# Kernel tuning notes

Measured on AMD Instinct MI355X. Metric: run time of the kernel, lower is better.

## Reference

```python
import jax, jax.numpy as jnp
import numpy as np

B, L, H, NH = 2, 2048, 1024, 16
HD = H // NH  # head dim = 64


def setup_inputs() -> dict:
    key = jax.random.key(0)
    ks = jax.random.split(key, 8)
    s = 0.02  # small init scale for weights
    return {
        "q": jax.random.normal(ks[0], (B, L, H), jnp.float32),
        "k": jax.random.normal(ks[1], (B, L, H), jnp.float32),
        "v": jax.random.normal(ks[2], (B, L, H), jnp.float32),
        "attention_mask": jnp.zeros((B, NH, L, L), jnp.float32),
        "Wq": jax.random.normal(ks[3], (H, H), jnp.float32) * s,
        "bq": jnp.zeros((H,), jnp.float32),
        "Wk": jax.random.normal(ks[4], (H, H), jnp.float32) * s,
        "bk": jnp.zeros((H,), jnp.float32),
        "Wv": jax.random.normal(ks[5], (H, H), jnp.float32) * s,
        "bv": jnp.zeros((H,), jnp.float32),
        "Wo": jax.random.normal(ks[6], (H, H), jnp.float32) * s,
        "bo": jnp.zeros((H,), jnp.float32),
    }


def reference(q, k, v, attention_mask, Wq, bq, Wk, bk, Wv, bv, Wo, bo):
    # Conv1D (GPT-2 style) projections: x @ W + b
    query = q @ Wq + bq  # [B, L, H]
    key = k @ Wk + bk
    value = v @ Wv + bv
    # split heads -> [B, NH, L, HD]
    qh = query.reshape(B, L, NH, HD).transpose(0, 2, 1, 3)
    kh = key.reshape(B, L, NH, HD).transpose(0, 2, 1, 3)
    vh = value.reshape(B, L, NH, HD).transpose(0, 2, 1, 3)
    # scores: [B, NH, L, L]
    w = jnp.einsum("bhqd,bhkd->bhqk", qh, kh) / jnp.sqrt(jnp.float32(HD))
    w = w + attention_mask
    w = jax.nn.softmax(w, axis=-1)  # dropout p=0 -> identity
    out = jnp.einsum("bhqk,bhkd->bhqd", w, vh)  # [B, NH, L, HD]
    # merge heads -> [B, L, H]
    out = out.transpose(0, 2, 1, 3).reshape(B, L, H)
    return out @ Wo + bo
```

## Files before the change

kernel.cpp:

```cpp
#include <hip/hip_runtime.h>

#define NBATCH 2
#define LSEQ   2048
#define NH     16
#define HD     64
#define HDIM   1024
#define MTOK   4096

typedef unsigned short u16;
typedef __attribute__((ext_vector_type(8))) short bf16x8;
typedef __attribute__((ext_vector_type(4))) float f32x4;

__device__ __forceinline__ u16 f2bf(float f) {
  union { float f; unsigned int u; } x; x.f = f;
  return (u16)((x.u + 0x7fffu + ((x.u >> 16) & 1u)) >> 16);
}

__device__ __forceinline__ void gload_lds16(const void* g, void* l) {
  __builtin_amdgcn_global_load_lds(
      (const __attribute__((address_space(1))) unsigned int*)g,
      (__attribute__((address_space(3))) unsigned int*)l, 16, 0, 0);
}

__global__ void prep_kernel(
    const float* __restrict__ q, const float* __restrict__ k, const float* __restrict__ v,
    const float* __restrict__ W0, const float* __restrict__ W1,
    const float* __restrict__ W2, const float* __restrict__ W3,
    u16* __restrict__ xq, u16* __restrict__ xk, u16* __restrict__ xv,
    u16* __restrict__ T0, u16* __restrict__ T1, u16* __restrict__ T2,
    u16* __restrict__ T3) {
  __shared__ float tile[64][65];
  if (blockIdx.z < 3) {
    const float* in = (blockIdx.z == 0) ? q : (blockIdx.z == 1) ? k : v;
    u16* out = (blockIdx.z == 0) ? xq : (blockIdx.z == 1) ? xk : xv;
    int i = blockIdx.x * blockDim.x + threadIdx.x;
    float4 t4 = ((const float4*)in)[i];
    ushort4 o;
    o.x = f2bf(t4.x); o.y = f2bf(t4.y); o.z = f2bf(t4.z); o.w = f2bf(t4.w);
    ((ushort4*)out)[i] = o;
    return;
  }
  if (blockIdx.x >= 1024) return;
  const int sel = blockIdx.x >> 8, bx = blockIdx.x & 255;
  const float* W = (sel == 0) ? W0 : (sel == 1) ? W1 : (sel == 2) ? W2 : W3;
  u16* Wt = (sel == 0) ? T0 : (sel == 1) ? T1 : (sel == 2) ? T2 : T3;
  const int k0 = (bx & 15) << 6;
  const int n0 = (bx >> 4) << 6;
  const int t = threadIdx.x;
#pragma unroll
  for (int i = 0; i < 4; ++i) {
    int idx = t + i * 256;
    int r = idx >> 4, c = (idx & 15) << 2;
    float4 v4 = *(const float4*)&W[(size_t)(k0 + r) * HDIM + n0 + c];
    tile[r][c] = v4.x; tile[r][c + 1] = v4.y; tile[r][c + 2] = v4.z; tile[r][c + 3] = v4.w;
  }
  __syncthreads();
#pragma unroll
  for (int i = 0; i < 4; ++i) {
    int idx = t + i * 256;
    int r = idx >> 4, c = (idx & 15) << 2;
    ushort4 o;
    o.x = f2bf(tile[c][r]);     o.y = f2bf(tile[c + 1][r]);
    o.z = f2bf(tile[c + 2][r]); o.w = f2bf(tile[c + 3][r]);
    *(ushort4*)&Wt[(size_t)(n0 + r) * HDIM + k0 + c] = o;
  }
}

template <int MODE>
__device__ __forceinline__ void gemm_core(u16* As, u16* Bs, int m0, int n0,
    const u16* __restrict__ A, const u16* __restrict__ Bt,
    const float* __restrict__ bias, void* __restrict__ Cout) {
  const int tid = threadIdx.x;
  const int lane = tid & 63, wid = tid >> 6;
  const int l15 = lane & 15, g = lane >> 4;
  const int wr = wid >> 1, wc = wid & 1;
  f32x4 acc[4][4];
#pragma unroll
  for (int i = 0; i < 4; ++i)
#pragma unroll
    for (int j = 0; j < 4; ++j) acc[i][j] = (f32x4){0.f, 0.f, 0.f, 0.f};

  for (int t = 0; t < HDIM / 64; ++t) {
    const int k0 = t * 64;
    __syncthreads();
#pragma unroll
    for (int i = 0; i < 4; ++i) {
      const int row = wid * 32 + i * 8 + (lane >> 3);
      const int colb = (lane & 7) * 16;
      gload_lds16((const char*)(A + (size_t)(m0 + row) * HDIM + k0) + colb,
                  (char*)As + (wid * 32 + i * 8) * 128);
      gload_lds16((const char*)(Bt + (size_t)(n0 + row) * HDIM + k0) + colb,
                  (char*)Bs + (wid * 32 + i * 8) * 128);
    }
    __syncthreads();
#pragma unroll
    for (int ks = 0; ks < 2; ++ks) {
      bf16x8 a[4], b[4];
#pragma unroll
      for (int i = 0; i < 4; ++i) {
        const int row = wr * 64 + i * 16 + l15;
        a[i] = *(const bf16x8*)((const char*)As + row * 128 + ks * 64 + g * 16);
      }
#pragma unroll
      for (int j = 0; j < 4; ++j) {
        const int row = wc * 64 + j * 16 + l15;
        b[j] = *(const bf16x8*)((const char*)Bs + row * 128 + ks * 64 + g * 16);
      }
#pragma unroll
      for (int i = 0; i < 4; ++i)
#pragma unroll
        for (int j = 0; j < 4; ++j)
          acc[i][j] = __builtin_amdgcn_mfma_f32_16x16x32_bf16(a[i], b[j], acc[i][j], 0, 0, 0);
    }
  }
#pragma unroll
  for (int i = 0; i < 4; ++i) {
    const int mrow = m0 + wr * 64 + i * 16 + 4 * g;
#pragma unroll
    for (int j = 0; j < 4; ++j) {
      const int ncol = n0 + wc * 64 + j * 16 + l15;
      const float bb = bias[ncol];
      if (MODE == 3) {
        float* o = (float*)Cout;
#pragma unroll
        for (int r = 0; r < 4; ++r)
          o[(size_t)(mrow + r) * HDIM + ncol] = acc[i][j][r] + bb;
      } else if (MODE == 2) {
        const int bidx = mrow >> 11, l0 = mrow & (LSEQ - 1);
        const int h = ncol >> 6, d = ncol & 63;
        ushort4 o4;
        o4.x = f2bf(acc[i][j][0] + bb); o4.y = f2bf(acc[i][j][1] + bb);
        o4.z = f2bf(acc[i][j][2] + bb); o4.w = f2bf(acc[i][j][3] + bb);
        *(ushort4*)&((u16*)Cout)[(((size_t)bidx * NH + h) * HD + d) * LSEQ + l0] = o4;
      } else {
        const int h = ncol >> 6, d = ncol & 63;
        u16* o = (u16*)Cout;
#pragma unroll
        for (int r = 0; r < 4; ++r) {
          const int m = mrow + r;
          const int bidx = m >> 11, l = m & (LSEQ - 1);
          o[(((size_t)bidx * NH + h) * LSEQ + l) * HD + d] = f2bf(acc[i][j][r] + bb);
        }
      }
    }
  }
}

__global__ __launch_bounds__(256, 3) void proj_gemm_kernel(
    const u16* __restrict__ xq, const u16* __restrict__ xk, const u16* __restrict__ xv,
    const u16* __restrict__ WqT, const u16* __restrict__ WkT, const u16* __restrict__ WvT,
    const float* __restrict__ bq, const float* __restrict__ bk, const float* __restrict__ bv,
    u16* __restrict__ Qh, u16* __restrict__ Kh, u16* __restrict__ Vt) {
  __shared__ u16 As[128 * 64];
  __shared__ u16 Bs[128 * 64];
  const int h = blockIdx.x;
  const int l = (h & 7) * 96 + (h >> 3);
  const int z = l >> 8, rem = l & 255;
  const int m0 = (rem >> 3) * 128, n0 = (rem & 7) * 128;
  if (z == 0)      gemm_core<0>(As, Bs, m0, n0, xq, WqT, bq, Qh);
  else if (z == 1) gemm_core<0>(As, Bs, m0, n0, xk, WkT, bk, Kh);
  else             gemm_core<2>(As, Bs, m0, n0, xv, WvT, bv, Vt);
}

__global__ __launch_bounds__(256, 3) void out_gemm_kernel(
    const u16* __restrict__ A, const u16* __restrict__ WoT,
    const float* __restrict__ bo, float* __restrict__ out) {
  __shared__ u16 As[128 * 64];
  __shared__ u16 Bs[128 * 64];
  const int h = blockIdx.x;
  const int l = (h & 7) * 32 + (h >> 3);
  const int m0 = (l >> 3) * 128, n0 = (l & 7) * 128;
  gemm_core<3>(As, Bs, m0, n0, A, WoT, bo, out);
}

__global__ __launch_bounds__(256, 4) void attn_kernel(
    const u16* __restrict__ Qh, const u16* __restrict__ Kh,
    const u16* __restrict__ Vt, const float* __restrict__ mask,
    u16* __restrict__ Out ) {
  __shared__ u16 Ks[2][64 * 64];
  __shared__ u16 Vs[2][64 * 64];
  __shared__ u16 Ps[4][16 * 64];
  const int lane = threadIdx.x & 63, w = threadIdx.x >> 6;
  const int l15 = lane & 15, g = lane >> 4;
  const int kk = blockIdx.x >> 3, xcd = blockIdx.x & 7;
  const int bh = xcd * 4 + (kk >> 5);
  const int qb = kk & 31;
  const int q0 = qb * 64 + w * 16;
  const int NT = LSEQ / 64;

  bf16x8 aq[2];
  {
    const u16* qbase = Qh + ((size_t)bh * LSEQ + q0 + l15) * HD;
    aq[0] = *(const bf16x8*)(qbase + g * 8);
    aq[1] = *(const bf16x8*)(qbase + 32 + g * 8);
  }
  f32x4 o_acc[4];
#pragma unroll
  for (int db = 0; db < 4; ++db) o_acc[db] = (f32x4){0.f, 0.f, 0.f, 0.f};
  float m_run = -1e30f, l_run = 0.f;

  const size_t kbase = (size_t)bh * LSEQ * HD;
  const size_t vbase = (size_t)bh * HD * LSEQ;
  const int srow = w * 16 + (lane >> 3);
  const int scolb = (lane & 7) * 16;

#define STAGE(buf, tt) do {                                                    \
    const int kv0_ = (tt) * 64;                                                \
    _Pragma("unroll")                                                          \
    for (int i_ = 0; i_ < 2; ++i_) {                                           \
      const int row_ = srow + i_ * 8;                                          \
      const int cb_ = scolb ^ ((row_ & 7) << 4);                               \
      gload_lds16((const char*)(Kh + kbase + (size_t)(kv0_ + row_) * HD) + cb_,\
                  (char*)Ks[buf] + (w * 16 + i_ * 8) * 128);                   \
      gload_lds16((const char*)(Vt + vbase + (size_t)row_ * LSEQ + kv0_) + cb_,\
                  (char*)Vs[buf] + (w * 16 + i_ * 8) * 128);                   \
    }                                                                          \
  } while (0)

  const float* mrow = mask + ((size_t)bh * LSEQ + q0 + l15) * LSEQ;
  f32x4 mvA[4], mvB[4];

  STAGE(0, 0);
#pragma unroll
  for (int mb = 0; mb < 4; ++mb) {
    mvA[mb] = *(const f32x4*)(mrow + 0 * 64 + mb * 16 + 4 * g);
    mvB[mb] = *(const f32x4*)(mrow + 1 * 64 + mb * 16 + 4 * g);
  }
  __syncthreads();

  u16* pbase = Ps[w];
  const int srcbase = (lane & 48) | ((lane & 48) >> 2);
  const int pswz = (l15 & 7) << 4;

#define TILE_BODY(t, cur, mv) do {                                            \
    if ((t) + 1 < NT) STAGE((cur) ^ 1, (t) + 1);                              \
               \
    f32x4 s_acc[4];                                                           \
    _Pragma("unroll")                                                         \
    for (int mb = 0; mb < 4; ++mb) s_acc[mb] = (f32x4){0.f, 0.f, 0.f, 0.f};   \
    __builtin_amdgcn_s_setprio(1);                                            \
    _Pragma("unroll")                                                         \
    for (int ks = 0; ks < 2; ++ks) {                                          \
      _Pragma("unroll")                                                       \
      for (int mb = 0; mb < 4; ++mb) {                                        \
        const int row = mb * 16 + l15;                                        \
        bf16x8 bk = *(const bf16x8*)((const char*)Ks[cur] + row * 128 +       \
                                     ((ks * 64 + g * 16) ^ ((row & 7) << 4)));\
        s_acc[mb] = __builtin_amdgcn_mfma_f32_16x16x32_bf16(bk, aq[ks],       \
                                                            s_acc[mb], 0,0,0);\
      }                                                                       \
    }                                                                         \
    __builtin_amdgcn_s_setprio(0);                                            \
                              \
    float p[4][4];                                                            \
    float tmax = -1e30f;                                                      \
    _Pragma("unroll")                                                         \
    for (int mb = 0; mb < 4; ++mb)                                            \
      _Pragma("unroll")                                                       \
      for (int r = 0; r < 4; ++r) {                                           \
        p[mb][r] = s_acc[mb][r] * 0.125f + mv[mb][r];                         \
        tmax = fmaxf(tmax, p[mb][r]);                                         \
      }                                                                       \
    tmax = fmaxf(tmax, __shfl_xor(tmax, 16));                                 \
    tmax = fmaxf(tmax, __shfl_xor(tmax, 32));                                 \
    if (!__all(tmax - m_run <= 8.f)) {                     \
      const float mnew = fmaxf(m_run, tmax);                                  \
      const float cf = __expf(m_run - mnew);                                  \
      m_run = mnew;                                                           \
      l_run *= cf;                                                            \
      float cfr[4];                                                           \
      _Pragma("unroll")                                                       \
      for (int r = 0; r < 4; ++r) cfr[r] = __shfl(cf, srcbase + r);           \
      _Pragma("unroll")                                                       \
      for (int db = 0; db < 4; ++db)                                          \
        _Pragma("unroll")                                                     \
        for (int r = 0; r < 4; ++r) o_acc[db][r] *= cfr[r];                   \
    }                                                                         \
    float psum = 0.f;                                                         \
    _Pragma("unroll")                                                         \
    for (int mb = 0; mb < 4; ++mb)                                            \
      _Pragma("unroll")                                                       \
      for (int r = 0; r < 4; ++r) {                                           \
        p[mb][r] = __expf(p[mb][r] - m_run);                                  \
        psum += p[mb][r];                                                     \
      }                                                                       \
    psum += __shfl_xor(psum, 16);                                             \
    psum += __shfl_xor(psum, 32);                                             \
    l_run += psum;                                                            \
                             \
    _Pragma("unroll")                                                         \
    for (int mb = 0; mb < 4; ++mb) {                                          \
      ushort4 pk;                                                             \
      pk.x = f2bf(p[mb][0]); pk.y = f2bf(p[mb][1]);                           \
      pk.z = f2bf(p[mb][2]); pk.w = f2bf(p[mb][3]);                           \
      *(ushort4*)((char*)pbase + l15 * 128 + ((mb * 32 + 8 * g) ^ pswz)) = pk;\
    }                                                                         \
           \
    __builtin_amdgcn_sched_barrier(0);                                        \
    {                                                                         \
      const int tn = ((t) + 2 < NT) ? (t) + 2 : NT - 1;                       \
      const float* mnext = mrow + tn * 64;                                    \
      _Pragma("unroll")                                                       \
      for (int mb = 0; mb < 4; ++mb)                                          \
        mv[mb] = *(const f32x4*)(mnext + mb * 16 + 4 * g);                    \
    }                                                                         \
                      \
    asm volatile("s_waitcnt lgkmcnt(0)" ::: "memory");                        \
    __builtin_amdgcn_sched_barrier(0);                                        \
                                                                \
    __builtin_amdgcn_s_setprio(1);                                            \
    _Pragma("unroll")                                                         \
    for (int s = 0; s < 2; ++s) {                                             \
      bf16x8 pa = *(const bf16x8*)((const char*)pbase + l15 * 128 +           \
                                   ((s * 64 + 16 * g) ^ pswz));               \
      _Pragma("unroll")                                                       \
      for (int db = 0; db < 4; ++db) {                                        \
        const int row = db * 16 + l15;                                        \
        bf16x8 bv = *(const bf16x8*)((const char*)Vs[cur] + row * 128 +       \
                                     ((s * 64 + 16 * g) ^ ((row & 7) << 4))); \
        o_acc[db] = __builtin_amdgcn_mfma_f32_16x16x32_bf16(pa, bv,           \
                                                            o_acc[db], 0,0,0);\
      }                                                                       \
    }                                                                         \
    __builtin_amdgcn_s_setprio(0);                                            \
         \
    asm volatile("s_waitcnt vmcnt(4)" ::: "memory");                          \
    __builtin_amdgcn_s_barrier();                                             \
    __builtin_amdgcn_sched_barrier(0);                                        \
  } while (0)

  for (int t = 0; t < NT; t += 2) {
    TILE_BODY(t, 0, mvA);
    TILE_BODY(t + 1, 1, mvB);
  }
#undef TILE_BODY
#undef STAGE

  const int b = bh >> 4, h = bh & 15;
  float lr[4];
#pragma unroll
  for (int r = 0; r < 4; ++r) lr[r] = __shfl(l_run, srcbase + r);
#pragma unroll
  for (int r = 0; r < 4; ++r) {
    const float inv = 1.f / lr[r];
    const int qg = q0 + 4 * g + r;
    u16* orow = Out + ((size_t)(b * LSEQ + qg) * NH + h) * HD;
#pragma unroll
    for (int db = 0; db < 4; ++db)
      orow[db * 16 + l15] = f2bf(o_acc[db][r] * inv);
  }
}

extern "C" void kernel_launch(void* const* d_in, const int* in_sizes, int n_in,
                              void* d_out, int out_size, void* d_ws, size_t ws_size,
                              hipStream_t stream) {
  (void)in_sizes; (void)n_in; (void)out_size; (void)ws_size;
  const float* q    = (const float*)d_in[0];
  const float* k    = (const float*)d_in[1];
  const float* v    = (const float*)d_in[2];
  const float* mask = (const float*)d_in[3];
  const float* Wq   = (const float*)d_in[4];
  const float* bq   = (const float*)d_in[5];
  const float* Wk   = (const float*)d_in[6];
  const float* bk   = (const float*)d_in[7];
  const float* Wv   = (const float*)d_in[8];
  const float* bv   = (const float*)d_in[9];
  const float* Wo   = (const float*)d_in[10];
  const float* bo   = (const float*)d_in[11];
  float* out = (float*)d_out;

  char* ws = (char*)d_ws;
  const size_t XB = (size_t)MTOK * HDIM * 2;
  const size_t WB = (size_t)HDIM * HDIM * 2;
  u16* xq   = (u16*)(ws);
  u16* xk   = (u16*)(ws + XB);
  u16* xv   = (u16*)(ws + 2 * XB);
  u16* WqT  = (u16*)(ws + 3 * XB);
  u16* WkT  = (u16*)(ws + 3 * XB + WB);
  u16* WvT  = (u16*)(ws + 3 * XB + 2 * WB);
  u16* WoT  = (u16*)(ws + 3 * XB + 3 * WB);
  u16* Qh   = (u16*)(ws + 3 * XB + 4 * WB);
  u16* Kh   = (u16*)(ws + 4 * XB + 4 * WB);
  u16* Vt   = (u16*)(ws + 5 * XB + 4 * WB);
  u16* aout = (u16*)(ws + 6 * XB + 4 * WB);

  prep_kernel<<<dim3((MTOK * HDIM) / 4 / 256, 1, 4), 256, 0, stream>>>(
      q, k, v, Wq, Wk, Wv, Wo, xq, xk, xv, WqT, WkT, WvT, WoT);
  proj_gemm_kernel<<<768, 256, 0, stream>>>(
      xq, xk, xv, WqT, WkT, WvT, bq, bk, bv, Qh, Kh, Vt);
  attn_kernel<<<1024, 256, 0, stream>>>(Qh, Kh, Vt, mask, aout);
  out_gemm_kernel<<<256, 256, 0, stream>>>(aout, WoT, bo, out);
}
```

Baseline: 226.5 us.

## Load K/V tiles directly from global into registers, drop LDS staging

Removes the LDS double-buffered K and V staging (global_load_lds plus block barriers) and has each wave load its K and V MFMA operands straight from global memory into registers every tile. Launch bounds drop from 4 to 2 blocks per SM to make room for the extra registers. This removes block-wide synchronisation and LDS traffic. In exchange, each of the 4 waves now fetches the same K/V data from global/L2 (4x redundancy), loads are no longer prefetched a tile ahead, and occupancy is lower.

```diff
diff --git a/kernel.cpp b/kernel.cpp
--- a/kernel.cpp
+++ b/kernel.cpp
@@ -173,12 +173,10 @@
   gemm_core<3>(As, Bs, m0, n0, A, WoT, bo, out);
 }
 
-__global__ __launch_bounds__(256, 4) void attn_kernel(
+__global__ __launch_bounds__(256, 2) void attn_kernel(
     const u16* __restrict__ Qh, const u16* __restrict__ Kh,
     const u16* __restrict__ Vt, const float* __restrict__ mask,
     u16* __restrict__ Out ) {
-  __shared__ u16 Ks[2][64 * 64];
-  __shared__ u16 Vs[2][64 * 64];
   __shared__ u16 Ps[4][16 * 64];
   const int lane = threadIdx.x & 63, w = threadIdx.x >> 6;
   const int l15 = lane & 15, g = lane >> 4;
@@ -199,58 +197,49 @@
   for (int db = 0; db < 4; ++db) o_acc[db] = (f32x4){0.f, 0.f, 0.f, 0.f};
   float m_run = -1e30f, l_run = 0.f;
 
-  const size_t kbase = (size_t)bh * LSEQ * HD;
-  const size_t vbase = (size_t)bh * HD * LSEQ;
-  const int srow = w * 16 + (lane >> 3);
-  const int scolb = (lane & 7) * 16;
-
-#define STAGE(buf, tt) do {                                                    \
-    const int kv0_ = (tt) * 64;                                                \
-    _Pragma("unroll")                                                          \
-    for (int i_ = 0; i_ < 2; ++i_) {                                           \
-      const int row_ = srow + i_ * 8;                                          \
-      const int cb_ = scolb ^ ((row_ & 7) << 4);                               \
-      gload_lds16((const char*)(Kh + kbase + (size_t)(kv0_ + row_) * HD) + cb_,\
-                  (char*)Ks[buf] + (w * 16 + i_ * 8) * 128);                   \
-      gload_lds16((const char*)(Vt + vbase + (size_t)row_ * LSEQ + kv0_) + cb_,\
-                  (char*)Vs[buf] + (w * 16 + i_ * 8) * 128);                   \
-    }                                                                          \
-  } while (0)
+  const u16* kbase = Kh + (size_t)bh * LSEQ * HD + (size_t)l15 * HD + g * 8;
+  const u16* vbase = Vt + (size_t)bh * HD * LSEQ + (size_t)l15 * LSEQ + g * 8;
 
   const float* mrow = mask + ((size_t)bh * LSEQ + q0 + l15) * LSEQ;
   f32x4 mvA[4], mvB[4];
-
-  STAGE(0, 0);
 #pragma unroll
   for (int mb = 0; mb < 4; ++mb) {
     mvA[mb] = *(const f32x4*)(mrow + 0 * 64 + mb * 16 + 4 * g);
     mvB[mb] = *(const f32x4*)(mrow + 1 * 64 + mb * 16 + 4 * g);
   }
-  __syncthreads();
 
   u16* pbase = Ps[w];
   const int srcbase = (lane & 48) | ((lane & 48) >> 2);
   const int pswz = (l15 & 7) << 4;
 
-#define TILE_BODY(t, cur, mv) do {                                            \
-    if ((t) + 1 < NT) STAGE((cur) ^ 1, (t) + 1);                              \
-               \
+#define TILE_BODY(t, mv) do {                                                 \
+    const u16* kp = kbase + (size_t)((t) * 64) * HD;                          \
+                                  \
+    bf16x8 bks[2][4];                                                         \
+    _Pragma("unroll")                                                         \
+    for (int ks = 0; ks < 2; ++ks)                                            \
+      _Pragma("unroll")                                                       \
+      for (int mb = 0; mb < 4; ++mb)                                          \
+        bks[ks][mb] = *(const bf16x8*)(kp + (size_t)mb * 16 * HD + ks * 32);  \
     f32x4 s_acc[4];                                                           \
     _Pragma("unroll")                                                         \
     for (int mb = 0; mb < 4; ++mb) s_acc[mb] = (f32x4){0.f, 0.f, 0.f, 0.f};   \
     __builtin_amdgcn_s_setprio(1);                                            \
     _Pragma("unroll")                                                         \
-    for (int ks = 0; ks < 2; ++ks) {                                          \
-      _Pragma("unroll")                                                       \
-      for (int mb = 0; mb < 4; ++mb) {                                        \
-        const int row = mb * 16 + l15;                                        \
-        bf16x8 bk = *(const bf16x8*)((const char*)Ks[cur] + row * 128 +       \
-                                     ((ks * 64 + g * 16) ^ ((row & 7) << 4)));\
-        s_acc[mb] = __builtin_amdgcn_mfma_f32_16x16x32_bf16(bk, aq[ks],       \
-                                                            s_acc[mb], 0,0,0);\
-      }                                                                       \
-    }                                                                         \
+    for (int ks = 0; ks < 2; ++ks)                                            \
+      _Pragma("unroll")                                                       \
+      for (int mb = 0; mb < 4; ++mb)                                          \
+        s_acc[mb] = __builtin_amdgcn_mfma_f32_16x16x32_bf16(bks[ks][mb],      \
+                                                 aq[ks], s_acc[mb], 0, 0, 0); \
     __builtin_amdgcn_s_setprio(0);                                            \
+           \
+    bf16x8 bvs[2][4];                                                         \
+    _Pragma("unroll")                                                         \
+    for (int s = 0; s < 2; ++s)                                               \
+      _Pragma("unroll")                                                       \
+      for (int db = 0; db < 4; ++db)                                          \
+        bvs[s][db] = *(const bf16x8*)(vbase + (size_t)db * 16 * LSEQ +        \
+                                      (t) * 64 + s * 32);                     \
                               \
     float p[4][4];                                                            \
     float tmax = -1e30f;                                                      \
@@ -287,7 +276,7 @@
     psum += __shfl_xor(psum, 16);                                             \
     psum += __shfl_xor(psum, 32);                                             \
     l_run += psum;                                                            \
-                             \
+           \
     _Pragma("unroll")                                                         \
     for (int mb = 0; mb < 4; ++mb) {                                          \
       ushort4 pk;                                                             \
@@ -295,8 +284,7 @@
       pk.z = f2bf(p[mb][2]); pk.w = f2bf(p[mb][3]);                           \
       *(ushort4*)((char*)pbase + l15 * 128 + ((mb * 32 + 8 * g) ^ pswz)) = pk;\
     }                                                                         \
-           \
-    __builtin_amdgcn_sched_barrier(0);                                        \
+                                \
     {                                                                         \
       const int tn = ((t) + 2 < NT) ? (t) + 2 : NT - 1;                       \
       const float* mnext = mrow + tn * 64;                                    \
@@ -304,7 +292,7 @@
       for (int mb = 0; mb < 4; ++mb)                                          \
         mv[mb] = *(const f32x4*)(mnext + mb * 16 + 4 * g);                    \
     }                                                                         \
-                      \
+          \
     asm volatile("s_waitcnt lgkmcnt(0)" ::: "memory");                        \
     __builtin_amdgcn_sched_barrier(0);                                        \
                                                                 \
@@ -314,27 +302,18 @@
       bf16x8 pa = *(const bf16x8*)((const char*)pbase + l15 * 128 +           \
                                    ((s * 64 + 16 * g) ^ pswz));               \
       _Pragma("unroll")                                                       \
-      for (int db = 0; db < 4; ++db) {                                        \
-        const int row = db * 16 + l15;                                        \
-        bf16x8 bv = *(const bf16x8*)((const char*)Vs[cur] + row * 128 +       \
-                                     ((s * 64 + 16 * g) ^ ((row & 7) << 4))); \
-        o_acc[db] = __builtin_amdgcn_mfma_f32_16x16x32_bf16(pa, bv,           \
+      for (int db = 0; db < 4; ++db)                                          \
+        o_acc[db] = __builtin_amdgcn_mfma_f32_16x16x32_bf16(pa, bvs[s][db],   \
                                                             o_acc[db], 0,0,0);\
-      }                                                                       \
     }                                                                         \
     __builtin_amdgcn_s_setprio(0);                                            \
-         \
-    asm volatile("s_waitcnt vmcnt(4)" ::: "memory");                          \
-    __builtin_amdgcn_s_barrier();                                             \
-    __builtin_amdgcn_sched_barrier(0);                                        \
   } while (0)
 
   for (int t = 0; t < NT; t += 2) {
-    TILE_BODY(t, 0, mvA);
-    TILE_BODY(t + 1, 1, mvB);
+    TILE_BODY(t, mvA);
+    TILE_BODY(t + 1, mvB);
   }
 #undef TILE_BODY
-#undef STAGE
 
   const int b = bh >> 4, h = bh & 15;
   float lr[4];
```

Result: slower. 377.1 us (+66.5%).
